# Optimization experiments

Measured on AMD Instinct MI355X. Metric: run time of the kernel, lower is better.

The kernel has to match this reference:

```python
import jax, jax.numpy as jnp
import numpy as np

H_DIM = 64
GRID = 8
NS = 2.0  # neighborhood_size


def _pool_seq(hidden, pos):
    # hidden: (P, H_DIM) hidden states of peds in one scene; pos: (P, 2) end positions
    P = hidden.shape[0]
    g2 = GRID * GRID
    tl_x = pos[:, 0] - NS / 2
    tl_y = pos[:, 1] + NS / 2
    br_x = pos[:, 0] + NS / 2
    br_y = pos[:, 1] - NS / 2
    # pair (i, j): grid of ped i (rows), position of ped j (cols)
    ox = pos[None, :, 0]
    oy = pos[None, :, 1]
    cell_x = jnp.floor((ox - tl_x[:, None]) / NS * GRID)
    cell_y = jnp.floor((tl_y[:, None] - oy) / NS * GRID)
    grid_pos = (cell_x + cell_y * GRID).astype(jnp.int32)
    # out-of-bound if outside neighborhood box OR i == j (diagonal forced out)
    oob = ((ox >= br_x[:, None]) | (ox <= tl_x[:, None])
           | (oy >= tl_y[:, None]) | (oy <= br_y[:, None])
           | jnp.eye(P, dtype=bool))
    idx = grid_pos + 1 + (jnp.arange(P, dtype=jnp.int32) * g2)[:, None]
    idx = jnp.where(oob, 0, idx)  # slot 0 is the trash bin (dropped below)
    src = jnp.broadcast_to(hidden[None], (P, P, H_DIM)).reshape(P * P, H_DIM)
    buf = jnp.zeros((P * g2 + 1, H_DIM), hidden.dtype)
    buf = buf.at[idx.reshape(-1)].add(src)
    return buf[1:].reshape(P, g2 * H_DIM)


def reference(h_states, seq_start_end, end_pos, rel_pos, W, b):
    B = end_pos.shape[0]
    S = seq_start_end.shape[0]
    P = B // S  # equal-length scenes -> static reshape
    hidden = h_states.reshape(-1, H_DIM).reshape(S, P, H_DIM)
    pos = end_pos.reshape(S, P, 2)
    pooled = jax.vmap(_pool_seq)(hidden, pos).reshape(B, GRID * GRID * H_DIM)
    # make_mlp([4096, 1024], relu, batch_norm=False): Linear -> ReLU
    return jax.nn.relu(pooled @ W + b)


def setup_inputs():
    key = jax.random.key(0)
    k0, k1, k2, k3 = jax.random.split(key, 4)
    S, P = 64, 64
    B = S * P
    bottleneck = 1024
    feat = GRID * GRID * H_DIM  # 4096
    h_states = jax.random.normal(k0, (1, B, H_DIM), jnp.float32)
    starts = jnp.arange(S, dtype=jnp.int32) * P
    seq_start_end = jnp.stack([starts, starts + P], axis=1)
    end_pos = jax.random.normal(k1, (B, 2), jnp.float32)
    rel_pos = jax.random.normal(k2, (B, 2), jnp.float32)
    W = jax.random.normal(k3, (feat, bottleneck), jnp.float32) * 0.02
    b = jnp.zeros((bottleneck,), jnp.float32)
    return {"h_states": h_states, "seq_start_end": seq_start_end,
            "end_pos": end_pos, "rel_pos": rel_pos, "W": W, "b": b}
```

## Files before the change

### kernel.cpp

```cpp
#include <hip/hip_runtime.h>


#define BM 128
#define BN 128
#define BK 64

typedef short short8 __attribute__((ext_vector_type(8)));
typedef short short4v __attribute__((ext_vector_type(4)));
typedef float floatx16 __attribute__((ext_vector_type(16)));

__device__ inline short f2bf(float x) {
    union { float f; unsigned u; } v; v.f = x;
    unsigned r = v.u + 0x7fffu + ((v.u >> 16) & 1u);
    return (short)(r >> 16);
}

__device__ inline void gload_lds16(const void* g, void* l) {
    __builtin_amdgcn_global_load_lds(
        (const __attribute__((address_space(1))) void*)g,
        (__attribute__((address_space(3))) void*)l,
        16, 0, 0);
}

__global__ __launch_bounds__(256) void prep_kernel(
    const float* __restrict__ h,
    const float* __restrict__ pos,
    short* __restrict__ pooled,
    const float* __restrict__ W,
    short* __restrict__ Wt,
    int K, int N, int poolBlocks)
{
    __shared__ __align__(16) unsigned char sh[18944];
    const int tid = threadIdx.x;

    if ((int)blockIdx.x < poolBlocks) {
        float* hs = (float*)sh;
        float* px = (float*)(sh + 16384);
        float* py = (float*)(sh + 16640);
        unsigned long long* wmask = (unsigned long long*)(sh + 16896);

        const int lane = tid & 63;
        const int w    = tid >> 6;
        const int s    = blockIdx.x >> 4;
        const int grp  = blockIdx.x & 15;
        const size_t base = (size_t)s * 64;

        const float4* hv  = (const float4*)(h + base * 64);
        float4*       hsv = (float4*)hs;
        #pragma unroll
        for (int c = 0; c < 4; ++c) hsv[tid + c * 256] = hv[tid + c * 256];
        if (tid < 64) {
            float2 p = ((const float2*)pos)[base + tid];
            px[tid] = p.x; py[tid] = p.y;
        }
        wmask[w * 64 + lane] = 0ull;
        __syncthreads();

        const int i = grp * 4 + w;
        const float tlx = px[i] - 1.0f;
        const float tly = py[i] + 1.0f;
        const float brx = px[i] + 1.0f;
        const float bry = py[i] - 1.0f;

        {
            const int j = lane;
            const float ox = px[j], oy = py[j];
            if (ox < brx && ox > tlx && oy < tly && oy > bry && j != i) {
                int cx = (int)floorf((ox - tlx) * 4.0f);
                int cy = (int)floorf((tly - oy) * 4.0f);
                atomicOr(&wmask[w * 64 + cx + cy * 8], 1ull << j);
            }
        }

        const int d = lane;
        const size_t orow = (base + i) * 4096;
        for (int c = 0; c < 64; ++c) {
            unsigned long long m = wmask[w * 64 + c];
            float a0 = 0.f, a1 = 0.f;
            while (m) {
                int j0 = __builtin_ctzll(m); m &= m - 1;
                if (m) {
                    int j1 = __builtin_ctzll(m); m &= m - 1;
                    a1 += hs[j1 * 64 + d];
                }
                a0 += hs[j0 * 64 + d];
            }
            pooled[orow + c * 64 + d] = f2bf(a0 + a1);
        }
    } else {
        float* t = (float*)sh;
        const int bid = blockIdx.x - poolBlocks;
        const int k0 = (bid & 63) * 64;
        const int n0 = (bid >> 6) * 64;

        const int r  = tid >> 4;
        const int cq = (tid & 15) * 4;
        #pragma unroll
        for (int i2 = 0; i2 < 4; ++i2) {
            const int row = r + i2 * 16;
            float4 v = *(const float4*)&W[(size_t)(k0 + row) * N + n0 + cq];
            t[row * 65 + cq + 0] = v.x; t[row * 65 + cq + 1] = v.y;
            t[row * 65 + cq + 2] = v.z; t[row * 65 + cq + 3] = v.w;
        }
        __syncthreads();
        const int nl = tid >> 4;
        const int kq = (tid & 15) * 4;
        #pragma unroll
        for (int i2 = 0; i2 < 4; ++i2) {
            const int n = nl + i2 * 16;
            short4v o;
            o.x = f2bf(t[(kq + 0) * 65 + n]); o.y = f2bf(t[(kq + 1) * 65 + n]);
            o.z = f2bf(t[(kq + 2) * 65 + n]); o.w = f2bf(t[(kq + 3) * 65 + n]);
            *(short4v*)&Wt[(size_t)(n0 + n) * K + k0 + kq] = o;
        }
    }
}

__global__ __launch_bounds__(256) void gemm_bias_relu(
    const short* __restrict__ A,
    const short* __restrict__ Bt,
    const float* __restrict__ bias,
    float* __restrict__ out,
    int M, int N, int K)
{
    __shared__ __align__(16) short smem[2][2][BM * BK];

    const int tid  = threadIdx.x;
    const int lane = tid & 63;
    const int wave = tid >> 6;
    const int wr = wave >> 1;
    const int wc = wave & 1;
    const int nl = lane & 31;
    const int hl = lane >> 5;
    const int k7 = nl & 7;

    const int b  = blockIdx.x;
    const int ib = b >> 3;
    const int m0 = ((b & 7) * 4 + (ib >> 3)) * BM;
    const int n0 = (ib & 7) * BN;

    const int r8    = lane >> 3;
    const int slot3 = lane & 7;

    const short* ag[4];
    const short* bg[4];
    #pragma unroll
    for (int c = 0; c < 4; ++c) {
        const int g  = c * 4 + wave;
        const int rl = g * 8 + r8;
        ag[c] = A  + (size_t)(m0 + rl) * K + (slot3 ^ (rl & 7)) * 8;
        bg[c] = Bt + (size_t)(n0 + rl) * K + (slot3 ^ (rl & 7)) * 8;
    }

    floatx16 acc[2][2];
    #pragma unroll
    for (int i = 0; i < 2; ++i)
        #pragma unroll
        for (int j = 0; j < 2; ++j)
            #pragma unroll
            for (int r = 0; r < 16; ++r) acc[i][j][r] = 0.f;

    #pragma unroll
    for (int c = 0; c < 4; ++c) {
        gload_lds16(ag[c], &smem[0][0][(c * 4 + wave) * 512]);
        gload_lds16(bg[c], &smem[0][1][(c * 4 + wave) * 512]);
        ag[c] += BK; bg[c] += BK;
    }
    __syncthreads();

    for (int kb = 0; kb < K; kb += BK) {
        const int bu = (kb >> 6) & 1;
        if (kb + BK < K) {
            #pragma unroll
            for (int c = 0; c < 4; ++c) {
                gload_lds16(ag[c], &smem[bu ^ 1][0][(c * 4 + wave) * 512]);
                gload_lds16(bg[c], &smem[bu ^ 1][1][(c * 4 + wave) * 512]);
                ag[c] += BK; bg[c] += BK;
            }
        }
        #pragma unroll
        for (int t = 0; t < 4; ++t) {
            const int g = 2 * t + hl;
            const int go = (g ^ k7) * 8;
            short8 a0 = *(const short8*)&smem[bu][0][(wr * 64 +      nl) * BK + go];
            short8 a1 = *(const short8*)&smem[bu][0][(wr * 64 + 32 + nl) * BK + go];
            short8 b0 = *(const short8*)&smem[bu][1][(wc * 64 +      nl) * BK + go];
            short8 b1 = *(const short8*)&smem[bu][1][(wc * 64 + 32 + nl) * BK + go];
            acc[0][0] = __builtin_amdgcn_mfma_f32_32x32x16_bf16(a0, b0, acc[0][0], 0, 0, 0);
            acc[0][1] = __builtin_amdgcn_mfma_f32_32x32x16_bf16(a0, b1, acc[0][1], 0, 0, 0);
            acc[1][0] = __builtin_amdgcn_mfma_f32_32x32x16_bf16(a1, b0, acc[1][0], 0, 0, 0);
            acc[1][1] = __builtin_amdgcn_mfma_f32_32x32x16_bf16(a1, b1, acc[1][1], 0, 0, 0);
        }
        __syncthreads();
    }

    #pragma unroll
    for (int jt = 0; jt < 2; ++jt) {
        const int gn = n0 + wc * 64 + jt * 32 + nl;
        const float bv = bias[gn];
        #pragma unroll
        for (int mt = 0; mt < 2; ++mt) {
            #pragma unroll
            for (int r = 0; r < 16; ++r) {
                const int row32 = (r & 3) + 8 * (r >> 2) + 4 * hl;
                const int gm = m0 + wr * 64 + mt * 32 + row32;
                float v = acc[mt][jt][r] + bv;
                out[(size_t)gm * N + gn] = v > 0.f ? v : 0.f;
            }
        }
    }
}

extern "C" void kernel_launch(void* const* d_in, const int* in_sizes, int n_in,
                              void* d_out, int out_size, void* d_ws, size_t ws_size,
                              hipStream_t stream) {
    const float* h    = (const float*)d_in[0];
    const float* pos  = (const float*)d_in[2];
    const float* W    = (const float*)d_in[4];
    const float* bias = (const float*)d_in[5];

    const int B = in_sizes[0] / 64;
    const int N = in_sizes[5];
    const int K = 64 * 64;

    short* pooled = (short*)d_ws;
    short* Wt     = pooled + (size_t)B * K;
    float* out    = (float*)d_out;

    const int poolBlocks = B / 4;
    const int castBlocks = (K / 64) * (N / 64);
    prep_kernel<<<poolBlocks + castBlocks, 256, 0, stream>>>(
        h, pos, pooled, W, Wt, K, N, poolBlocks);
    gemm_bias_relu<<<(B / BM) * (N / BN), 256, 0, stream>>>(
        pooled, Wt, bias, out, B, N, K);
}
```

Measured before the change: 135.6 us.

## Split GEMM K-loop across two wave groups with LDS reduction at epilogue

The GEMM block grows from 256 to 512 threads. Two groups of four waves each handle half of every BK=64 slice of K, using the same 128x128 output tile and accumulators per wave. A new LDS layout packs two rows per 128-short line with an XOR swizzle. At the end, group 1 writes its partial sums to LDS and group 0 adds them, applies bias and ReLU, and stores. The goal is more waves per CU to hide latency, at the cost of a cross-group reduction and heavier register pressure under launch_bounds(512,2).

```diff
diff --git a/kernel.cpp b/kernel.cpp
--- a/kernel.cpp
+++ b/kernel.cpp
@@ -116,40 +116,44 @@
     }
 }
 
-__global__ __launch_bounds__(256) void gemm_bias_relu(
+__global__ __launch_bounds__(512, 2) void gemm_bias_relu(
     const short* __restrict__ A,
     const short* __restrict__ Bt,
     const float* __restrict__ bias,
     float* __restrict__ out,
     int M, int N, int K)
 {
-    __shared__ __align__(16) short smem[2][2][BM * BK];
+    __shared__ __align__(16) short smem[2][2][64 * 128];
 
     const int tid  = threadIdx.x;
     const int lane = tid & 63;
     const int wave = tid >> 6;
-    const int wr = wave >> 1;
-    const int wc = wave & 1;
+    const int kg = wave >> 2;
+    const int w4 = wave & 3;
+    const int wr = w4 >> 1;
+    const int wc = w4 & 1;
     const int nl = lane & 31;
     const int hl = lane >> 5;
-    const int k7 = nl & 7;
+    const int key = (nl >> 1) & 7;
 
     const int b  = blockIdx.x;
     const int ib = b >> 3;
     const int m0 = ((b & 7) * 4 + (ib >> 3)) * BM;
     const int n0 = (ib & 7) * BN;
 
-    const int r8    = lane >> 3;
-    const int slot3 = lane & 7;
-
-    const short* ag[4];
-    const short* bg[4];
+    const short* ag[2];
+    const short* bg[2];
+    int cpr[2];
     #pragma unroll
-    for (int c = 0; c < 4; ++c) {
-        const int g  = c * 4 + wave;
-        const int rl = g * 8 + r8;
-        ag[c] = A  + (size_t)(m0 + rl) * K + (slot3 ^ (rl & 7)) * 8;
-        bg[c] = Bt + (size_t)(n0 + rl) * K + (slot3 ^ (rl & 7)) * 8;
+    for (int c = 0; c < 2; ++c) {
+        const int cp = c * 8 + wave;
+        const int R  = cp * 4 + (lane >> 4);
+        const int s  = lane & 15;
+        const int rl = 2 * R + (s >> 3);
+        const int g  = (s & 7) ^ (R & 7);
+        cpr[c] = cp;
+        ag[c] = A  + (size_t)(m0 + rl) * K + g * 8;
+        bg[c] = Bt + (size_t)(n0 + rl) * K + g * 8;
     }
 
     floatx16 acc[2][2];
@@ -161,52 +165,77 @@
             for (int r = 0; r < 16; ++r) acc[i][j][r] = 0.f;
 
     #pragma unroll
-    for (int c = 0; c < 4; ++c) {
-        gload_lds16(ag[c], &smem[0][0][(c * 4 + wave) * 512]);
-        gload_lds16(bg[c], &smem[0][1][(c * 4 + wave) * 512]);
+    for (int c = 0; c < 2; ++c) {
+        gload_lds16(ag[c], &smem[0][0][cpr[c] * 512]);
+        gload_lds16(bg[c], &smem[0][1][cpr[c] * 512]);
         ag[c] += BK; bg[c] += BK;
     }
     __syncthreads();
 
-    for (int kb = 0; kb < K; kb += BK) {
-        const int bu = (kb >> 6) & 1;
-        if (kb + BK < K) {
-            #pragma unroll
-            for (int c = 0; c < 4; ++c) {
-                gload_lds16(ag[c], &smem[bu ^ 1][0][(c * 4 + wave) * 512]);
-                gload_lds16(bg[c], &smem[bu ^ 1][1][(c * 4 + wave) * 512]);
+    const int nIter = K / BK;
+    for (int it = 0; it < nIter; ++it) {
+        const int bu = it & 1;
+        if (it + 1 < nIter) {
+            #pragma unroll
+            for (int c = 0; c < 2; ++c) {
+                gload_lds16(ag[c], &smem[bu ^ 1][0][cpr[c] * 512]);
+                gload_lds16(bg[c], &smem[bu ^ 1][1][cpr[c] * 512]);
                 ag[c] += BK; bg[c] += BK;
             }
         }
         #pragma unroll
-        for (int t = 0; t < 4; ++t) {
-            const int g = 2 * t + hl;
-            const int go = (g ^ k7) * 8;
-            short8 a0 = *(const short8*)&smem[bu][0][(wr * 64 +      nl) * BK + go];
-            short8 a1 = *(const short8*)&smem[bu][0][(wr * 64 + 32 + nl) * BK + go];
-            short8 b0 = *(const short8*)&smem[bu][1][(wc * 64 +      nl) * BK + go];
-            short8 b1 = *(const short8*)&smem[bu][1][(wc * 64 + 32 + nl) * BK + go];
-            acc[0][0] = __builtin_amdgcn_mfma_f32_32x32x16_bf16(a0, b0, acc[0][0], 0, 0, 0);
-            acc[0][1] = __builtin_amdgcn_mfma_f32_32x32x16_bf16(a0, b1, acc[0][1], 0, 0, 0);
-            acc[1][0] = __builtin_amdgcn_mfma_f32_32x32x16_bf16(a1, b0, acc[1][0], 0, 0, 0);
-            acc[1][1] = __builtin_amdgcn_mfma_f32_32x32x16_bf16(a1, b1, acc[1][1], 0, 0, 0);
+        for (int t = 0; t < 2; ++t) {
+            const int g = kg * 4 + 2 * t + hl;
+            const int so = ((g ^ key) & 7) * 8;
+            short8 af[2], bf[2];
+            #pragma unroll
+            for (int mt = 0; mt < 2; ++mt) {
+                const int R = wr * 32 + mt * 16 + (nl >> 1);
+                af[mt] = *(const short8*)&smem[bu][0][R * 128 + (nl & 1) * 64 + so];
+            }
+            #pragma unroll
+            for (int jt = 0; jt < 2; ++jt) {
+                const int R = wc * 32 + jt * 16 + (nl >> 1);
+                bf[jt] = *(const short8*)&smem[bu][1][R * 128 + (nl & 1) * 64 + so];
+            }
+            #pragma unroll
+            for (int mt = 0; mt < 2; ++mt)
+                #pragma unroll
+                for (int jt = 0; jt < 2; ++jt)
+                    acc[mt][jt] = __builtin_amdgcn_mfma_f32_32x32x16_bf16(
+                        af[mt], bf[jt], acc[mt][jt], 0, 0, 0);
         }
         __syncthreads();
     }
 
-    #pragma unroll
-    for (int jt = 0; jt < 2; ++jt) {
-        const int gn = n0 + wc * 64 + jt * 32 + nl;
-        const float bv = bias[gn];
-        #pragma unroll
-        for (int mt = 0; mt < 2; ++mt) {
-            #pragma unroll
-            for (int r = 0; r < 16; ++r) {
-                const int row32 = (r & 3) + 8 * (r >> 2) + 4 * hl;
-                const int gm = m0 + wr * 64 + mt * 32 + row32;
-                float v = acc[mt][jt][r] + bv;
-                out[(size_t)gm * N + gn] = v > 0.f ? v : 0.f;
-            }
+    float* xp = (float*)smem + w4 * 4096;
+    if (kg == 1) {
+        #pragma unroll
+        for (int mt = 0; mt < 2; ++mt)
+            #pragma unroll
+            for (int jt = 0; jt < 2; ++jt)
+                #pragma unroll
+                for (int r = 0; r < 16; ++r) {
+                    const int row = mt * 32 + (r & 3) + 8 * (r >> 2) + 4 * hl;
+                    const int col = jt * 32 + nl;
+                    xp[row * 64 + col] = acc[mt][jt][r];
+                }
+    }
+    __syncthreads();
+    if (kg == 0) {
+        #pragma unroll
+        for (int jt = 0; jt < 2; ++jt) {
+            const int gn = n0 + wc * 64 + jt * 32 + nl;
+            const float bv = bias[gn];
+            #pragma unroll
+            for (int mt = 0; mt < 2; ++mt)
+                #pragma unroll
+                for (int r = 0; r < 16; ++r) {
+                    const int row = mt * 32 + (r & 3) + 8 * (r >> 2) + 4 * hl;
+                    float v = acc[mt][jt][r] + xp[row * 64 + jt * 32 + nl] + bv;
+                    const int gm = m0 + wr * 64 + row;
+                    out[(size_t)gm * N + gn] = v > 0.f ? v : 0.f;
+                }
         }
     }
 }
@@ -231,6 +260,6 @@
     const int castBlocks = (K / 64) * (N / 64);
     prep_kernel<<<poolBlocks + castBlocks, 256, 0, stream>>>(
         h, pos, pooled, W, Wt, K, N, poolBlocks);
-    gemm_bias_relu<<<(B / BM) * (N / BN), 256, 0, stream>>>(
+    gemm_bias_relu<<<(B / BM) * (N / BN), 512, 0, stream>>>(
         pooled, Wt, bias, out, B, N, K);
 }
```

Measured after the change: 137.6 us. No clear change (+1.4%).
